# Kernel tuning notes

Hardware: AMD Instinct MI355X
Metric: run time of the kernel (lower is better)

The kernel has to match this reference:

```python
import jax, jax.numpy as jnp
from jax import lax
import numpy as np

EPS = 1e-6

def setup_inputs() -> dict:
    key = jax.random.key(0)
    ks = jax.random.split(key, 6)
    b, c, h, w = 16, 512, 64, 64
    x = jax.random.normal(ks[0], (b, c, h, w), dtype=jnp.float32)
    s = jax.random.normal(ks[1], (b, c, 1, h * w), dtype=jnp.float32)
    z = jax.random.uniform(ks[2], (b, 1, c, 1), dtype=jnp.float32)
    wq = jax.random.normal(ks[3], (1, 1, 5), dtype=jnp.float32) * 0.2
    wk = jax.random.normal(ks[4], (1, 1, 5), dtype=jnp.float32) * 0.2
    wv = jax.random.normal(ks[5], (512, 1, 3, 3), dtype=jnp.float32) * 0.2
    return {"x": x, "s": s, "z": z, "wq": wq, "wk": wk, "wv": wv}

def _elu_fm(t):
    # elu feature map: elu(t) + 1 (strictly positive)
    return jax.nn.elu(t) + 1.0

def reference(x, s, z, wq, wk, wv):
    b, c, h, w = x.shape
    # adaptive avg pool to 1x1 -> [b,1,c] channel descriptor
    y = jnp.mean(x, axis=(2, 3)).reshape(b, 1, c)
    # ECA-style conv1d over channel axis (kernel 5, SAME padding)
    Q = lax.conv_general_dilated(y, wq, (1,), [(2, 2)],
                                 dimension_numbers=("NCW", "OIW", "NCW"))
    K = lax.conv_general_dilated(y, wk, (1,), [(2, 2)],
                                 dimension_numbers=("NCW", "OIW", "NCW"))
    # depthwise 3x3 conv on V
    V = lax.conv_general_dilated(x, wv, (1, 1), [(1, 1), (1, 1)],
                                 dimension_numbers=("NCHW", "OIHW", "NCHW"),
                                 feature_group_count=c)
    Qf = _elu_fm(Q)[:, 0, :]          # [b, c]
    Kf = _elu_fm(K)[:, 0, :]          # [b, c]
    Vf = V.reshape(b, c, h * w)       # [b, c, hw]
    # KV outer product per channel (c-dim of K is size-1 in einsum, so scalar * row)
    s_new = s + (Kf[:, :, None] * Vf)[:, :, None, :]   # [b, c, 1, hw]
    z_new = z + Kf.reshape(b, 1, c, 1)                 # [b, 1, c, 1]
    qz = 1.0 / (Qf * (z_new[:, 0, :, 0] + EPS))        # [b, c]
    out = (Qf * qz)[:, :, None] * s_new[:, :, 0, :]    # [b, c, hw]
    return out.reshape(b, c, h, w), s_new, z_new
```

## Files before the change

### kernel.cpp

```cpp
#include <hip/hip_runtime.h>
#include <math.h>

#define EPS 1e-6f

typedef float __attribute__((ext_vector_type(4))) fx4;

__global__ __launch_bounds__(256) void mean_kernel(const float* __restrict__ x,
                                                   float* __restrict__ y) {
    int plane = blockIdx.x;
    const fx4* xp = (const fx4*)(x + (size_t)plane * 4096);
    int t = threadIdx.x;
    float sum = 0.f;
#pragma unroll
    for (int k = 0; k < 4; ++k) {
        fx4 v = xp[t + k * 256];
        sum += v.x + v.y + v.z + v.w;
    }
#pragma unroll
    for (int off = 32; off > 0; off >>= 1)
        sum += __shfl_down(sum, off, 64);
    __shared__ float lds[4];
    if ((t & 63) == 0) lds[t >> 6] = sum;
    __syncthreads();
    if (t == 0) {
        float s = lds[0] + lds[1] + lds[2] + lds[3];
        y[plane] = s * (1.0f / 4096.0f);
    }
}

__global__ __launch_bounds__(256) void fused_kernel(
    const float* __restrict__ x, const float* __restrict__ s,
    const float* __restrict__ z, const float* __restrict__ wq,
    const float* __restrict__ wk, const float* __restrict__ wv,
    const float* __restrict__ y, float* __restrict__ out,
    float* __restrict__ s_new, float* __restrict__ z_new) {
    __shared__ float tile[4096];

    int plane = blockIdx.x;
    int b = plane >> 9;
    int ch = plane & 511;
    int t = threadIdx.x;

    const fx4* xp4 = (const fx4*)(x + (size_t)plane * 4096);
    fx4* t4 = (fx4*)tile;
#pragma unroll
    for (int k = 0; k < 4; ++k) {
        fx4 v = __builtin_nontemporal_load(xp4 + t + k * 256);
        t4[t + k * 256] = v;
    }

    float q = 0.f, kk = 0.f;
#pragma unroll
    for (int i = 0; i < 5; ++i) {
        int cc = ch + i - 2;
        float yv = (cc >= 0 && cc < 512) ? y[b * 512 + cc] : 0.f;
        q += yv * wq[i];
        kk += yv * wk[i];
    }
    float qf = (q > 0.f) ? (q + 1.f) : expf(q);
    float kf = (kk > 0.f) ? (kk + 1.f) : expf(kk);
    float zn = z[plane] + kf;
    if (t == 0) z_new[plane] = zn;
    float fac = qf * (1.0f / (qf * (zn + EPS)));

    const float* wvp = wv + ch * 9;
    float w00 = wvp[0], w01 = wvp[1], w02 = wvp[2];
    float w10 = wvp[3], w11 = wvp[4], w12 = wvp[5];
    float w20 = wvp[6], w21 = wvp[7], w22 = wvp[8];

    __syncthreads();

    int ty = t >> 4;
    int tx = t & 15;
    int col0 = tx << 2;

    float lm = (col0 == 0) ? 0.f : 1.f;
    float rm = (col0 == 60) ? 0.f : 1.f;
    int li = (col0 == 0) ? 0 : col0 - 1;
    int ri = (col0 == 60) ? 63 : col0 + 4;

#pragma unroll
    for (int rr = 0; rr < 4; ++rr) {
        int row = ty + rr * 16;
        int rcB = row * 64;
        int rmB = (row == 0) ? rcB : rcB - 64;
        int rpB = (row == 63) ? rcB : rcB + 64;
        float tm = (row == 0) ? 0.f : 1.f;
        float bm = (row == 63) ? 0.f : 1.f;

        fx4 tq = *(const fx4*)(tile + rmB + col0);
        float t0 = tile[rmB + li] * (tm * lm);
        float t1 = tq.x * tm, t2 = tq.y * tm, t3 = tq.z * tm, t4v = tq.w * tm;
        float t5 = tile[rmB + ri] * (tm * rm);

        fx4 cq = *(const fx4*)(tile + rcB + col0);
        float c0 = tile[rcB + li] * lm;
        float c1 = cq.x, c2 = cq.y, c3 = cq.z, c4 = cq.w;
        float c5 = tile[rcB + ri] * rm;

        fx4 bq = *(const fx4*)(tile + rpB + col0);
        float b0 = tile[rpB + li] * (bm * lm);
        float b1 = bq.x * bm, b2 = bq.y * bm, b3 = bq.z * bm, b4 = bq.w * bm;
        float b5 = tile[rpB + ri] * (bm * rm);

        float v0 = t0 * w00 + t1 * w01 + t2 * w02 +
                   c0 * w10 + c1 * w11 + c2 * w12 +
                   b0 * w20 + b1 * w21 + b2 * w22;
        float v1 = t1 * w00 + t2 * w01 + t3 * w02 +
                   c1 * w10 + c2 * w11 + c3 * w12 +
                   b1 * w20 + b2 * w21 + b3 * w22;
        float v2 = t2 * w00 + t3 * w01 + t4v * w02 +
                   c2 * w10 + c3 * w11 + c4 * w12 +
                   b2 * w20 + b3 * w21 + b4 * w22;
        float v3 = t3 * w00 + t4v * w01 + t5 * w02 +
                   c3 * w10 + c4 * w11 + c5 * w12 +
                   b3 * w20 + b4 * w21 + b5 * w22;

        size_t off = (size_t)plane * 4096 + (size_t)rcB + col0;
        fx4 s4 = __builtin_nontemporal_load((const fx4*)(s + off));
        fx4 sn;
        sn.x = s4.x + kf * v0;
        sn.y = s4.y + kf * v1;
        sn.z = s4.z + kf * v2;
        sn.w = s4.w + kf * v3;
        __builtin_nontemporal_store(sn, (fx4*)(s_new + off));
        fx4 o;
        o.x = fac * sn.x;
        o.y = fac * sn.y;
        o.z = fac * sn.z;
        o.w = fac * sn.w;
        __builtin_nontemporal_store(o, (fx4*)(out + off));
    }
}

extern "C" void kernel_launch(void* const* d_in, const int* in_sizes, int n_in,
                              void* d_out, int out_size, void* d_ws,
                              size_t ws_size, hipStream_t stream) {
    const float* x  = (const float*)d_in[0];
    const float* s  = (const float*)d_in[1];
    const float* z  = (const float*)d_in[2];
    const float* wq = (const float*)d_in[3];
    const float* wk = (const float*)d_in[4];
    const float* wv = (const float*)d_in[5];

    float* out   = (float*)d_out;
    float* s_new = out + 33554432;
    float* z_new = s_new + 33554432;

    float* ws = (float*)d_ws;
    float* y  = ws;

    mean_kernel<<<8192, 256, 0, stream>>>(x, y);
    fused_kernel<<<8192, 256, 0, stream>>>(x, s, z, wq, wk, wv, y,
                                           out, s_new, z_new);
}
```

Baseline: 446.1 us.

## Merge mean and fused kernels into one cooperative persistent kernel with grid sync

Replaces the separate mean and fused kernels with a single cooperative kernel of 512 blocks, each handling 16 planes. Blocks first compute the per-plane means wave by wave, then meet at a grid-wide sync, then loop over their planes running the depthwise conv and update while prefetching s into registers. This removes one kernel launch and lets x possibly hit in cache on the second read. In exchange it adds a grid barrier, leaves fewer blocks in flight for a bandwidth-bound workload, and serialises the per-plane work inside each block.

```diff
diff --git a/kernel.cpp b/kernel.cpp
--- a/kernel.cpp
+++ b/kernel.cpp
@@ -1,135 +1,145 @@
 #include <hip/hip_runtime.h>
+#include <hip/hip_cooperative_groups.h>
 #include <math.h>
+
+namespace cg = cooperative_groups;
 
 #define EPS 1e-6f
 
 typedef float __attribute__((ext_vector_type(4))) fx4;
 
-__global__ __launch_bounds__(256) void mean_kernel(const float* __restrict__ x,
-                                                   float* __restrict__ y) {
-    int plane = blockIdx.x;
-    const fx4* xp = (const fx4*)(x + (size_t)plane * 4096);
-    int t = threadIdx.x;
-    float sum = 0.f;
-#pragma unroll
-    for (int k = 0; k < 4; ++k) {
-        fx4 v = xp[t + k * 256];
-        sum += v.x + v.y + v.z + v.w;
-    }
-#pragma unroll
-    for (int off = 32; off > 0; off >>= 1)
-        sum += __shfl_down(sum, off, 64);
-    __shared__ float lds[4];
-    if ((t & 63) == 0) lds[t >> 6] = sum;
-    __syncthreads();
-    if (t == 0) {
-        float s = lds[0] + lds[1] + lds[2] + lds[3];
-        y[plane] = s * (1.0f / 4096.0f);
-    }
-}
-
-__global__ __launch_bounds__(256) void fused_kernel(
+__global__ __launch_bounds__(256, 2) void mega_kernel(
     const float* __restrict__ x, const float* __restrict__ s,
     const float* __restrict__ z, const float* __restrict__ wq,
     const float* __restrict__ wk, const float* __restrict__ wv,
-    const float* __restrict__ y, float* __restrict__ out,
+    float* __restrict__ y, float* __restrict__ out,
     float* __restrict__ s_new, float* __restrict__ z_new) {
     __shared__ float tile[4096];
 
-    int plane = blockIdx.x;
-    int b = plane >> 9;
-    int ch = plane & 511;
     int t = threadIdx.x;
+    int wave = t >> 6;
+    int lane = t & 63;
+    int pbase = blockIdx.x << 4;
 
-    const fx4* xp4 = (const fx4*)(x + (size_t)plane * 4096);
-    fx4* t4 = (fx4*)tile;
 #pragma unroll
-    for (int k = 0; k < 4; ++k) {
-        fx4 v = __builtin_nontemporal_load(xp4 + t + k * 256);
-        t4[t + k * 256] = v;
+    for (int i = 0; i < 4; ++i) {
+        int plane = pbase + (wave << 2) + i;
+        const fx4* xp = (const fx4*)(x + (size_t)plane * 4096);
+        float sum = 0.f;
+#pragma unroll 8
+        for (int k = 0; k < 16; ++k) {
+            fx4 v = xp[lane + k * 64];
+            sum += v.x + v.y + v.z + v.w;
+        }
+#pragma unroll
+        for (int off = 32; off > 0; off >>= 1)
+            sum += __shfl_down(sum, off, 64);
+        if (lane == 0) y[plane] = sum * (1.0f / 4096.0f);
     }
 
-    float q = 0.f, kk = 0.f;
-#pragma unroll
-    for (int i = 0; i < 5; ++i) {
-        int cc = ch + i - 2;
-        float yv = (cc >= 0 && cc < 512) ? y[b * 512 + cc] : 0.f;
-        q += yv * wq[i];
-        kk += yv * wk[i];
-    }
-    float qf = (q > 0.f) ? (q + 1.f) : expf(q);
-    float kf = (kk > 0.f) ? (kk + 1.f) : expf(kk);
-    float zn = z[plane] + kf;
-    if (t == 0) z_new[plane] = zn;
-    float fac = qf * (1.0f / (qf * (zn + EPS)));
-
-    const float* wvp = wv + ch * 9;
-    float w00 = wvp[0], w01 = wvp[1], w02 = wvp[2];
-    float w10 = wvp[3], w11 = wvp[4], w12 = wvp[5];
-    float w20 = wvp[6], w21 = wvp[7], w22 = wvp[8];
-
-    __syncthreads();
+    cg::this_grid().sync();
 
     int ty = t >> 4;
     int tx = t & 15;
     int col0 = tx << 2;
-
     float lm = (col0 == 0) ? 0.f : 1.f;
     float rm = (col0 == 60) ? 0.f : 1.f;
     int li = (col0 == 0) ? 0 : col0 - 1;
     int ri = (col0 == 60) ? 63 : col0 + 4;
 
+    for (int ip = 0; ip < 16; ++ip) {
+        int plane = pbase + ip;
+        int b = plane >> 9;
+        int ch = plane & 511;
+
+        const fx4* xp4 = (const fx4*)(x + (size_t)plane * 4096);
+        fx4* t4 = (fx4*)tile;
 #pragma unroll
-    for (int rr = 0; rr < 4; ++rr) {
-        int row = ty + rr * 16;
-        int rcB = row * 64;
-        int rmB = (row == 0) ? rcB : rcB - 64;
-        int rpB = (row == 63) ? rcB : rcB + 64;
-        float tm = (row == 0) ? 0.f : 1.f;
-        float bm = (row == 63) ? 0.f : 1.f;
+        for (int k = 0; k < 4; ++k)
+            t4[t + k * 256] = __builtin_nontemporal_load(xp4 + t + k * 256);
 
-        fx4 tq = *(const fx4*)(tile + rmB + col0);
-        float t0 = tile[rmB + li] * (tm * lm);
-        float t1 = tq.x * tm, t2 = tq.y * tm, t3 = tq.z * tm, t4v = tq.w * tm;
-        float t5 = tile[rmB + ri] * (tm * rm);
+        fx4 spre[4];
+#pragma unroll
+        for (int rr = 0; rr < 4; ++rr) {
+            int row = ty + rr * 16;
+            spre[rr] = __builtin_nontemporal_load(
+                (const fx4*)(s + (size_t)plane * 4096 + row * 64 + col0));
+        }
 
-        fx4 cq = *(const fx4*)(tile + rcB + col0);
-        float c0 = tile[rcB + li] * lm;
-        float c1 = cq.x, c2 = cq.y, c3 = cq.z, c4 = cq.w;
-        float c5 = tile[rcB + ri] * rm;
+        float q = 0.f, kk = 0.f;
+#pragma unroll
+        for (int i = 0; i < 5; ++i) {
+            int cc = ch + i - 2;
+            float yv = (cc >= 0 && cc < 512) ? y[b * 512 + cc] : 0.f;
+            q += yv * wq[i];
+            kk += yv * wk[i];
+        }
+        float qf = (q > 0.f) ? (q + 1.f) : expf(q);
+        float kf = (kk > 0.f) ? (kk + 1.f) : expf(kk);
+        float zn = z[plane] + kf;
+        if (t == 0) z_new[plane] = zn;
+        float fac = qf * (1.0f / (qf * (zn + EPS)));
 
-        fx4 bq = *(const fx4*)(tile + rpB + col0);
-        float b0 = tile[rpB + li] * (bm * lm);
-        float b1 = bq.x * bm, b2 = bq.y * bm, b3 = bq.z * bm, b4 = bq.w * bm;
-        float b5 = tile[rpB + ri] * (bm * rm);
+        const float* wvp = wv + ch * 9;
+        float w00 = wvp[0], w01 = wvp[1], w02 = wvp[2];
+        float w10 = wvp[3], w11 = wvp[4], w12 = wvp[5];
+        float w20 = wvp[6], w21 = wvp[7], w22 = wvp[8];
 
-        float v0 = t0 * w00 + t1 * w01 + t2 * w02 +
-                   c0 * w10 + c1 * w11 + c2 * w12 +
-                   b0 * w20 + b1 * w21 + b2 * w22;
-        float v1 = t1 * w00 + t2 * w01 + t3 * w02 +
-                   c1 * w10 + c2 * w11 + c3 * w12 +
-                   b1 * w20 + b2 * w21 + b3 * w22;
-        float v2 = t2 * w00 + t3 * w01 + t4v * w02 +
-                   c2 * w10 + c3 * w11 + c4 * w12 +
-                   b2 * w20 + b3 * w21 + b4 * w22;
-        float v3 = t3 * w00 + t4v * w01 + t5 * w02 +
-                   c3 * w10 + c4 * w11 + c5 * w12 +
-                   b3 * w20 + b4 * w21 + b5 * w22;
+        __syncthreads();
 
-        size_t off = (size_t)plane * 4096 + (size_t)rcB + col0;
-        fx4 s4 = __builtin_nontemporal_load((const fx4*)(s + off));
-        fx4 sn;
-        sn.x = s4.x + kf * v0;
-        sn.y = s4.y + kf * v1;
-        sn.z = s4.z + kf * v2;
-        sn.w = s4.w + kf * v3;
-        __builtin_nontemporal_store(sn, (fx4*)(s_new + off));
-        fx4 o;
-        o.x = fac * sn.x;
-        o.y = fac * sn.y;
-        o.z = fac * sn.z;
-        o.w = fac * sn.w;
-        __builtin_nontemporal_store(o, (fx4*)(out + off));
+#pragma unroll
+        for (int rr = 0; rr < 4; ++rr) {
+            int row = ty + rr * 16;
+            int rcB = row * 64;
+            int rmB = (row == 0) ? rcB : rcB - 64;
+            int rpB = (row == 63) ? rcB : rcB + 64;
+            float tm = (row == 0) ? 0.f : 1.f;
+            float bm = (row == 63) ? 0.f : 1.f;
+
+            fx4 tq = *(const fx4*)(tile + rmB + col0);
+            float t0 = tile[rmB + li] * (tm * lm);
+            float t1 = tq.x * tm, t2 = tq.y * tm, t3 = tq.z * tm, t4v = tq.w * tm;
+            float t5 = tile[rmB + ri] * (tm * rm);
+
+            fx4 cq = *(const fx4*)(tile + rcB + col0);
+            float c0 = tile[rcB + li] * lm;
+            float c1 = cq.x, c2 = cq.y, c3 = cq.z, c4 = cq.w;
+            float c5 = tile[rcB + ri] * rm;
+
+            fx4 bq = *(const fx4*)(tile + rpB + col0);
+            float b0 = tile[rpB + li] * (bm * lm);
+            float b1 = bq.x * bm, b2 = bq.y * bm, b3 = bq.z * bm, b4 = bq.w * bm;
+            float b5 = tile[rpB + ri] * (bm * rm);
+
+            float v0 = t0 * w00 + t1 * w01 + t2 * w02 +
+                       c0 * w10 + c1 * w11 + c2 * w12 +
+                       b0 * w20 + b1 * w21 + b2 * w22;
+            float v1 = t1 * w00 + t2 * w01 + t3 * w02 +
+                       c1 * w10 + c2 * w11 + c3 * w12 +
+                       b1 * w20 + b2 * w21 + b3 * w22;
+            float v2 = t2 * w00 + t3 * w01 + t4v * w02 +
+                       c2 * w10 + c3 * w11 + c4 * w12 +
+                       b2 * w20 + b3 * w21 + b4 * w22;
+            float v3 = t3 * w00 + t4v * w01 + t5 * w02 +
+                       c3 * w10 + c4 * w11 + c5 * w12 +
+                       b3 * w20 + b4 * w21 + b5 * w22;
+
+            size_t off = (size_t)plane * 4096 + (size_t)rcB + col0;
+            fx4 s4 = spre[rr];
+            fx4 sn;
+            sn.x = s4.x + kf * v0;
+            sn.y = s4.y + kf * v1;
+            sn.z = s4.z + kf * v2;
+            sn.w = s4.w + kf * v3;
+            __builtin_nontemporal_store(sn, (fx4*)(s_new + off));
+            fx4 o;
+            o.x = fac * sn.x;
+            o.y = fac * sn.y;
+            o.z = fac * sn.z;
+            o.w = fac * sn.w;
+            __builtin_nontemporal_store(o, (fx4*)(out + off));
+        }
+        __syncthreads();
     }
 }
 
@@ -147,10 +157,11 @@
     float* s_new = out + 33554432;
     float* z_new = s_new + 33554432;
 
-    float* ws = (float*)d_ws;
-    float* y  = ws;
+    float* y = (float*)d_ws;
 
-    mean_kernel<<<8192, 256, 0, stream>>>(x, y);
-    fused_kernel<<<8192, 256, 0, stream>>>(x, s, z, wq, wk, wv, y,
-                                           out, s_new, z_new);
+    void* args[] = {(void*)&x, (void*)&s, (void*)&z, (void*)&wq, (void*)&wk,
+                    (void*)&wv, (void*)&y, (void*)&out, (void*)&s_new,
+                    (void*)&z_new};
+    hipLaunchCooperativeKernel((const void*)mega_kernel, dim3(512), dim3(256),
+                               args, 0, stream);
 }
```

Result: slower. 519.9 us (+16.5%).
